# Performance work log

Measured on AMD Instinct MI355X. Metric: run time of the kernel, lower is better.

## Reference

```python
import jax, jax.numpy as jnp
import numpy as np
import math

D = 32   # in_planes / d_model
T = 9    # num_contexts
L = 24   # token_len
H = 8    # nhead
HD = D // H
NEUMANN = 3
ALPHA = 0.9

def _lin(x, w, b):
    return x @ w.T + b

def _gelu(x):
    return jax.nn.gelu(x, approximate=False)

def reference(x, ln_g, ln_b, rp_w1, rp_b1, rp_w2, rp_b2, W_causal,
              mask_w, mask_b, val_w1, val_b1, val_w2, val_b2, fuse_gate,
              q_w, q_b, k_w, k_b, v_w, v_b, m_w, m_b,
              W_logit, W_ctx, rel_pos_bias, pre_prompt, conv_w, conv_b, p_w, p_b):
    b = x.shape[0]
    x_btlc = jnp.transpose(x, (0, 2, 3, 1))              # (b,t,l,c)
    # ---- rule pooling (LayerNorm -> Linear -> GELU -> Linear) ----
    pooled = x_btlc.mean(axis=(1, 2))                    # (b,c)
    mu = pooled.mean(-1, keepdims=True)
    var = pooled.var(-1, keepdims=True)
    pn = (pooled - mu) / jnp.sqrt(var + 1e-5) * ln_g + ln_b
    pooled_rule = _lin(_gelu(_lin(pn, rp_w1, rp_b1)), rp_w2, rp_b2)
    # ---- causal graph discovery ----
    A = jax.nn.softplus(W_causal) * (1.0 - jnp.eye(D, dtype=x.dtype))
    # ---- intervention engine ----
    x_obs = x_btlc.mean(axis=(1, 2))                     # (b,c)
    scale = jnp.clip(jnp.std(x_btlc, axis=(1, 2), ddof=1), 1e-3)  # torch unbiased std
    M = jax.nn.sigmoid(_lin(pooled_rule, mask_w, mask_b))
    v_raw = _lin(_gelu(_lin(pooled_rule, val_w1, val_b1)), val_w2, val_b2)
    v32 = jnp.tanh(v_raw) * scale + x_obs
    x_do = (1.0 - M) * x_obs + M * v32
    A32 = ALPHA * A / (A.sum(-1, keepdims=True) + 1e-6)  # row-normalize
    y = x_do
    for _ in range(NEUMANN):                             # fp32 Neumann series
        y = x_do + y @ A32.T
    delta = (y - x_obs)[:, None, None, :]
    fused = x_btlc + jax.nn.sigmoid(fuse_gate) * delta   # (b,t,l,c)
    # ---- cosine-sim multi-head attention with rel-pos bias & head mixing ----
    def heads(w, bb):
        h = _lin(fused, w, bb).reshape(b, T, L, H, HD).transpose(0, 1, 3, 2, 4)
        return h / jnp.linalg.norm(h, axis=-1, keepdims=True).clip(1e-12)
    q = heads(q_w, q_b); k = heads(k_w, k_b); v = heads(v_w, v_b)
    logits = jnp.einsum('bthid,bthjd->bthij', q, k) / math.sqrt(HD)
    idx = jnp.arange(L)
    rel = jnp.clip(idx[:, None] - idx[None, :] + (L - 1), 0, 2 * L - 2)
    logits = logits + rel_pos_bias[:, rel][None, None]   # (h,L,L) broadcast
    logits = jnp.einsum('bthij,hH->btHij', logits, W_logit)
    atten = jax.nn.softmax(logits, axis=-1)
    atten = jnp.einsum('bthij,hH->btHij', atten, W_ctx)
    x_att = jnp.einsum('bthij,bthjd->bthid', atten, v)
    x_att = _lin(x_att.transpose(0, 1, 3, 2, 4).reshape(b, T, L, D), m_w, m_b)
    x_att = jnp.transpose(x_att, (0, 3, 1, 2))           # (b,c,t,l)
    # ---- prediction branch (conv over contexts + linear over tokens) ----
    pre = jnp.broadcast_to(pre_prompt, (b, D, 1, L))
    con = jnp.concatenate([x_att[:, :, :T - 1], pre], axis=2)   # (b,c,T,L)
    p = jax.lax.conv_general_dilated(con, conv_w, (1, 1), 'VALID',
        dimension_numbers=('NCHW', 'OIHW', 'NCHW')) + conv_b[None, :, None, None]
    p = jax.nn.relu(p)                                   # ConvNormAct act; norm=identity at init
    p = _lin(p, p_w, p_b)                                # Linear(token_len, token_len)
    p = x_att[:, :, T - 1:] - p
    return jnp.concatenate([x_att[:, :, :T - 1], p], axis=2)


def setup_inputs() -> dict:
    key = jax.random.key(0)
    ks = jax.random.split(key, 24)
    B = 4096
    def r(i, sh, s=0.02):
        return jax.random.normal(ks[i], sh, jnp.float32) * s
    return dict(
        x=jax.random.normal(ks[0], (B, D, T, L), jnp.float32),
        ln_g=jnp.ones((D,), jnp.float32), ln_b=jnp.zeros((D,), jnp.float32),
        rp_w1=r(1, (D, D)), rp_b1=jnp.zeros((D,), jnp.float32),
        rp_w2=r(2, (D, D)), rp_b2=jnp.zeros((D,), jnp.float32),
        W_causal=r(3, (D, D)),
        mask_w=r(4, (D, D)), mask_b=jnp.zeros((D,), jnp.float32),
        val_w1=r(5, (D, D)), val_b1=jnp.zeros((D,), jnp.float32),
        val_w2=r(6, (D, D)), val_b2=jnp.zeros((D,), jnp.float32),
        fuse_gate=jnp.float32(0.5),
        q_w=r(7, (D, D)), q_b=jnp.zeros((D,), jnp.float32),
        k_w=r(8, (D, D)), k_b=jnp.zeros((D,), jnp.float32),
        v_w=r(9, (D, D)), v_b=jnp.zeros((D,), jnp.float32),
        m_w=r(10, (D, D)), m_b=jnp.zeros((D,), jnp.float32),
        W_logit=jnp.eye(H, dtype=jnp.float32) + r(11, (H, H), 0.01),
        W_ctx=jnp.eye(H, dtype=jnp.float32) + r(12, (H, H), 0.01),
        rel_pos_bias=r(13, (H, 2 * L - 1)),
        pre_prompt=r(14, (1, D, 1, L)),
        conv_w=r(15, (D, D, T, 1)), conv_b=jnp.zeros((D,), jnp.float32),
        p_w=r(16, (L, L)), p_b=jnp.zeros((L,), jnp.float32),
    )
```

## Files before the change

kernel.cpp:

```cpp
#include <hip/hip_runtime.h>
#include <hip/hip_bf16.h>

#define DD 32
#define TT 9
#define LL 24
#define HH 8
#define NPOS 216
#define RPB_W 47
#define ALPHA 0.9f

__device__ __forceinline__ float gelu_exact(float x) {
    return 0.5f * x * (1.0f + erff(x * 0.7071067811865476f));
}
__device__ __forceinline__ float sigmoidf_(float x) { return 1.0f / (1.0f + expf(-x)); }


__global__ void k0_prep(const float* __restrict__ wcausal,
                        const float* __restrict__ w_logit,
                        const float* __restrict__ rpb,
                        float* __restrict__ ws) {
    __shared__ float A[DD][DD];
    __shared__ float rs[DD];
    int tid = threadIdx.x;
    int i = tid >> 5, j = tid & 31;
    float a = (i == j) ? 0.0f : log1pf(expf(wcausal[tid]));
    A[i][j] = a;
    __syncthreads();
    if (j == 0) {
        float s = 0.0f;
        for (int k = 0; k < DD; k++) s += A[i][k];
        rs[i] = ALPHA / (s + 1e-6f);
    }
    __syncthreads();
    ws[tid] = A[i][j] * rs[i];
    if (tid < 64) ws[1024 + tid] = 0.5f * w_logit[tid];
    if (tid < 384) {
        int H = tid / 48, r = tid % 48;
        float v = 0.0f;
        if (r < RPB_W) {
            for (int h = 0; h < HH; h++) v += w_logit[h * HH + H] * rpb[h * RPB_W + r];
        }
        ws[1088 + tid] = v;
    }
}

__global__ __launch_bounds__(256) void k1a(const float* __restrict__ x,
                                           float* __restrict__ sp, float* __restrict__ sq) {
    int b = blockIdx.x, tid = threadIdx.x;
    int c = tid >> 3, r = tid & 7;
    const float4* x4 = (const float4*)(x + (size_t)b * (DD * NPOS) + (size_t)c * NPOS);
    float s = 0.0f, q = 0.0f;
    for (int k = r; k < 54; k += 8) {
        float4 v = x4[k];
        s += v.x + v.y + v.z + v.w;
        q += v.x * v.x + v.y * v.y + v.z * v.z + v.w * v.w;
    }
    for (int m = 1; m < 8; m <<= 1) { s += __shfl_xor(s, m); q += __shfl_xor(q, m); }
    if (r == 0) { sp[b * DD + c] = s; sq[b * DD + c] = q; }
}

__global__ __launch_bounds__(64) void k1b(
    const float* __restrict__ ln_g, const float* __restrict__ ln_b,
    const float* __restrict__ rp_w1, const float* __restrict__ rp_b1,
    const float* __restrict__ rp_w2, const float* __restrict__ rp_b2,
    const float* __restrict__ mask_w, const float* __restrict__ mask_b,
    const float* __restrict__ val_w1, const float* __restrict__ val_b1,
    const float* __restrict__ val_w2, const float* __restrict__ val_b2,
    const float* __restrict__ fuse_gate, const float* __restrict__ ws,
    float* __restrict__ sp , const float* __restrict__ sq)
{
    __shared__ float W[6][1024];
    __shared__ float V[7][32];
    int tid = threadIdx.x;
    for (int idx = tid; idx < 1024; idx += 64) {
        W[0][idx] = rp_w1[idx]; W[1][idx] = rp_w2[idx]; W[2][idx] = mask_w[idx];
        W[3][idx] = val_w1[idx]; W[4][idx] = val_w2[idx]; W[5][idx] = ws[idx];
    }
    if (tid < 32) {
        V[0][tid] = ln_g[tid]; V[1][tid] = ln_b[tid]; V[2][tid] = rp_b1[tid];
        V[3][tid] = rp_b2[tid]; V[4][tid] = mask_b[tid]; V[5][tid] = val_b1[tid];
        V[6][tid] = val_b2[tid];
    }
    __syncthreads();
    int b = blockIdx.x * 64 + tid;

    float pooled[32], scl[32];
    const float4* sp4 = (const float4*)(sp + (size_t)b * 32);
    const float4* sq4 = (const float4*)(sq + (size_t)b * 32);
    #pragma unroll
    for (int k = 0; k < 8; k++) {
        float4 sv = sp4[k], qv = sq4[k];
        float ss[4] = {sv.x, sv.y, sv.z, sv.w};
        float qq[4] = {qv.x, qv.y, qv.z, qv.w};
        #pragma unroll
        for (int m = 0; m < 4; m++) {
            int c = 4 * k + m;
            float p = ss[m] * (1.0f / NPOS);
            pooled[c] = p;
            float var1 = (qq[m] - (float)NPOS * p * p) * (1.0f / (NPOS - 1));
            scl[c] = fmaxf(sqrtf(fmaxf(var1, 0.0f)), 1e-3f);
        }
    }
    float mu = 0.0f;
    #pragma unroll
    for (int c = 0; c < 32; c++) mu += pooled[c];
    mu *= (1.0f / 32.0f);
    float vv = 0.0f;
    #pragma unroll
    for (int c = 0; c < 32; c++) { float d = pooled[c] - mu; vv += d * d; }
    vv *= (1.0f / 32.0f);
    float inv = rsqrtf(vv + 1e-5f);
    float pn[32];
    #pragma unroll
    for (int c = 0; c < 32; c++) pn[c] = (pooled[c] - mu) * inv * V[0][c] + V[1][c];

    float h1[32];
    #pragma unroll
    for (int i = 0; i < 32; i++) {
        float acc = V[2][i];
        #pragma unroll
        for (int j = 0; j < 32; j++) acc += pn[j] * W[0][i * 32 + j];
        h1[i] = gelu_exact(acc);
    }
    float pr[32];
    #pragma unroll
    for (int i = 0; i < 32; i++) {
        float acc = V[3][i];
        #pragma unroll
        for (int j = 0; j < 32; j++) acc += h1[j] * W[1][i * 32 + j];
        pr[i] = acc;
    }
    float g1[32];
    #pragma unroll
    for (int i = 0; i < 32; i++) {
        float acc = V[5][i];
        #pragma unroll
        for (int j = 0; j < 32; j++) acc += pr[j] * W[3][i * 32 + j];
        g1[i] = gelu_exact(acc);
    }
    float xd[32];
    #pragma unroll
    for (int i = 0; i < 32; i++) {
        float am = V[4][i];
        #pragma unroll
        for (int j = 0; j < 32; j++) am += pr[j] * W[2][i * 32 + j];
        float M = sigmoidf_(am);
        float av = V[6][i];
        #pragma unroll
        for (int j = 0; j < 32; j++) av += g1[j] * W[4][i * 32 + j];
        float v32 = tanhf(av) * scl[i] + pooled[i];
        xd[i] = (1.0f - M) * pooled[i] + M * v32;
    }
    float y[32];
    #pragma unroll
    for (int c = 0; c < 32; c++) y[c] = xd[c];
    for (int it = 0; it < 3; it++) {
        float ny[32];
        #pragma unroll
        for (int i = 0; i < 32; i++) {
            float acc = xd[i];
            #pragma unroll
            for (int j = 0; j < 32; j++) acc += y[j] * W[5][i * 32 + j];
            ny[i] = acc;
        }
        #pragma unroll
        for (int c = 0; c < 32; c++) y[c] = ny[c];
    }
    float g = sigmoidf_(fuse_gate[0]);
    float4* dout4 = (float4*)(sp + (size_t)b * 32);
    #pragma unroll
    for (int k = 0; k < 8; k++) {
        float4 o;
        o.x = g * (y[4 * k + 0] - pooled[4 * k + 0]);
        o.y = g * (y[4 * k + 1] - pooled[4 * k + 1]);
        o.z = g * (y[4 * k + 2] - pooled[4 * k + 2]);
        o.w = g * (y[4 * k + 3] - pooled[4 * k + 3]);
        dout4[k] = o;
    }
}

__global__ __launch_bounds__(256) void k2_attn(
    const float* __restrict__ x,
    const float* __restrict__ ws,
    const float* __restrict__ delta,
    const float* __restrict__ q_w, const float* __restrict__ q_b,
    const float* __restrict__ k_w, const float* __restrict__ k_b,
    const float* __restrict__ v_w, const float* __restrict__ v_b,
    const float* __restrict__ m_w, const float* __restrict__ m_b,
    const float* __restrict__ w_ctx,
    float* __restrict__ out)
{
    __shared__ float r1[3456];
    __shared__ float r2[5824];
    __shared__ float msc[640];
    float* fusedf = r1;
    float* qsf = r1 + 864;
    float* ksf = r1 + 1728;
    float* vsf = r1 + 2592;
    float* wqf = r2;
    float* wkf = r2 + 1024;
    float* wvf = r2 + 2048;
    float* lgf = r2;
    float* wmf = r2 + 4800;
    float* bqf = msc, *bkf = msc + 32, *bvf = msc + 64, *bmf = msc + 96;
    float* wl05f = msc + 128;
    float* wcf = msc + 192;
    float* rpmf = msc + 256;

    int blk = blockIdx.x;
    int b = blk / TT, t = blk % TT;
    int tid = threadIdx.x;

    for (int idx = tid; idx < 768; idx += 256) {
        int m = idx >> 8, r = idx & 255;
        int i = r >> 3, jq = r & 7;
        const float* src = (m == 0) ? q_w : (m == 1) ? k_w : v_w;
        float* dst = (m == 0) ? wqf : (m == 1) ? wkf : wvf;
        float4 v = ((const float4*)src)[r];
        int col = i ^ (4 * jq);
        dst[(4 * jq + 0) * 32 + col] = v.x;
        dst[(4 * jq + 1) * 32 + col] = v.y;
        dst[(4 * jq + 2) * 32 + col] = v.z;
        dst[(4 * jq + 3) * 32 + col] = v.w;
    }
    if (tid < 32) { bqf[tid] = q_b[tid]; bkf[tid] = k_b[tid]; bvf[tid] = v_b[tid]; bmf[tid] = m_b[tid]; }
    else if (tid < 96) wl05f[tid - 32] = ws[1024 + tid - 32];
    else if (tid < 160) wcf[tid - 96] = w_ctx[tid - 96];
    for (int idx = tid; idx < 384; idx += 256) rpmf[idx] = ws[1088 + idx];
    if (tid < 192) {
        int c = tid / 6, k = tid % 6;
        const float4* p = (const float4*)(x + (size_t)b * (DD * NPOS) + (size_t)c * NPOS + t * LL);
        float4 v = p[k];
        float gd = delta[b * DD + c];
        int l0 = 4 * k;
        fusedf[(l0 + 0) * 36 + c] = v.x + gd;
        fusedf[(l0 + 1) * 36 + c] = v.y + gd;
        fusedf[(l0 + 2) * 36 + c] = v.z + gd;
        fusedf[(l0 + 3) * 36 + c] = v.w + gd;
    }
    __syncthreads();

    if (tid < 192) {
        int l = tid >> 3, q = tid & 7;
        float4 aq = *(const float4*)&bqf[4 * q];
        float4 ak = *(const float4*)&bkf[4 * q];
        float4 av = *(const float4*)&bvf[4 * q];
        #pragma unroll
        for (int j = 0; j < 32; j++) {
            float f = fusedf[l * 36 + j];
            int sw = (4 * q) ^ (j & 28);
            float4 w0 = *(const float4*)&wqf[j * 32 + sw];
            float4 w1 = *(const float4*)&wkf[j * 32 + sw];
            float4 w2 = *(const float4*)&wvf[j * 32 + sw];
            aq.x += f * w0.x; aq.y += f * w0.y; aq.z += f * w0.z; aq.w += f * w0.w;
            ak.x += f * w1.x; ak.y += f * w1.y; ak.z += f * w1.z; ak.w += f * w1.w;
            av.x += f * w2.x; av.y += f * w2.y; av.z += f * w2.z; av.w += f * w2.w;
        }
        float nq = 1.0f / fmaxf(sqrtf(aq.x*aq.x + aq.y*aq.y + aq.z*aq.z + aq.w*aq.w), 1e-12f);
        float nk = 1.0f / fmaxf(sqrtf(ak.x*ak.x + ak.y*ak.y + ak.z*ak.z + ak.w*ak.w), 1e-12f);
        float nv = 1.0f / fmaxf(sqrtf(av.x*av.x + av.y*av.y + av.z*av.z + av.w*av.w), 1e-12f);
        aq.x *= nq; aq.y *= nq; aq.z *= nq; aq.w *= nq;
        ak.x *= nk; ak.y *= nk; ak.z *= nk; ak.w *= nk;
        av.x *= nv; av.y *= nv; av.z *= nv; av.w *= nv;
        *(float4*)&qsf[l * 36 + 4 * q] = aq;
        *(float4*)&ksf[l * 36 + 4 * q] = ak;
        *(float4*)&vsf[l * 36 + 4 * q] = av;
    }
    __syncthreads();

    {
        int idx = tid;
        int i = idx >> 3, jq = idx & 7;
        float4 v = ((const float4*)m_w)[idx];
        int col = i ^ (4 * jq);
        wmf[(4 * jq + 0) * 32 + col] = v.x;
        wmf[(4 * jq + 1) * 32 + col] = v.y;
        wmf[(4 * jq + 2) * 32 + col] = v.z;
        wmf[(4 * jq + 3) * 32 + col] = v.w;
    }
    if (tid < 192) {
        int h = tid & 7, i2 = tid >> 3;
        float4 q4 = *(const float4*)&qsf[i2 * 36 + 4 * h];
        float row[24];
        #pragma unroll
        for (int j = 0; j < 24; j++) {
            float4 k4 = *(const float4*)&ksf[j * 36 + 4 * h];
            row[j] = q4.x * k4.x + q4.y * k4.y + q4.z * k4.z + q4.w * k4.w;
        }
        #pragma unroll
        for (int j = 0; j < 24; j++) lgf[h * 600 + i2 * 25 + j] = row[j];
    }
    __syncthreads();

    for (int ij = tid; ij < 576; ij += 256) {
        int i = ij / 24, j = ij - i * 24;
        int off = i * 25 + j;
        int rel = i - j + (LL - 1);
        float tmp[8];
        #pragma unroll
        for (int h = 0; h < 8; h++) tmp[h] = lgf[h * 600 + off];
        #pragma unroll
        for (int H = 0; H < 8; H++) {
            float a = rpmf[H * 48 + rel];
            #pragma unroll
            for (int h = 0; h < 8; h++) a += tmp[h] * wl05f[h * 8 + H];
            lgf[H * 600 + off] = a;
        }
    }
    __syncthreads();

    if (tid < 192) {
        int H = tid & 7, i = tid >> 3;
        float* rp = &lgf[H * 600 + i * 25];
        float mx = -1e30f;
        #pragma unroll
        for (int j = 0; j < 24; j++) mx = fmaxf(mx, rp[j]);
        float s = 0.0f;
        #pragma unroll
        for (int j = 0; j < 24; j++) { float e = __expf(rp[j] - mx); rp[j] = e; s += e; }
        float inv = 1.0f / s;
        #pragma unroll
        for (int j = 0; j < 24; j++) rp[j] *= inv;
    }
    __syncthreads();

    for (int ij = tid; ij < 576; ij += 256) {
        int i = ij / 24, j = ij - i * 24;
        int off = i * 25 + j;
        float tmp[8];
        #pragma unroll
        for (int h = 0; h < 8; h++) tmp[h] = lgf[h * 600 + off];
        #pragma unroll
        for (int H = 0; H < 8; H++) {
            float a = 0.0f;
            #pragma unroll
            for (int h = 0; h < 8; h++) a += tmp[h] * wcf[h * 8 + H];
            lgf[H * 600 + off] = a;
        }
    }
    __syncthreads();

    if (tid < 192) {
        int l = tid >> 3, q = tid & 7;
        float4 acc = {0.0f, 0.0f, 0.0f, 0.0f};
        #pragma unroll
        for (int j = 0; j < 24; j++) {
            float a = lgf[q * 600 + l * 25 + j];
            float4 v4 = *(const float4*)&vsf[j * 36 + 4 * q];
            acc.x += a * v4.x; acc.y += a * v4.y; acc.z += a * v4.z; acc.w += a * v4.w;
        }
        *(float4*)&fusedf[l * 36 + 4 * q] = acc;
    }
    __syncthreads();

    if (tid < 192) {
        int l = tid >> 3, q = tid & 7;
        float4 acc = *(const float4*)&bmf[4 * q];
        #pragma unroll
        for (int c = 0; c < 32; c++) {
            float f = fusedf[l * 36 + c];
            int sw = (4 * q) ^ (c & 28);
            float4 w4 = *(const float4*)&wmf[c * 32 + sw];
            acc.x += f * w4.x; acc.y += f * w4.y; acc.z += f * w4.z; acc.w += f * w4.w;
        }
        float* resf = qsf;
        resf[(4 * q + 0) * 25 + l] = acc.x;
        resf[(4 * q + 1) * 25 + l] = acc.y;
        resf[(4 * q + 2) * 25 + l] = acc.z;
        resf[(4 * q + 3) * 25 + l] = acc.w;
    }
    __syncthreads();

    if (tid < 192) {
        const float* resf = qsf;
        int c = tid / 6, k = tid - c * 6;
        float4 v;
        v.x = resf[c * 25 + 4 * k + 0];
        v.y = resf[c * 25 + 4 * k + 1];
        v.z = resf[c * 25 + 4 * k + 2];
        v.w = resf[c * 25 + 4 * k + 3];
        float4* o4 = (float4*)(out + (size_t)b * (DD * NPOS) + (size_t)c * NPOS + t * LL);
        o4[k] = v;
    }
}

__global__ __launch_bounds__(256) void k3_pred(
    const float* __restrict__ pre_prompt,
    const float* __restrict__ conv_w, const float* __restrict__ conv_b,
    const float* __restrict__ p_w, const float* __restrict__ p_b,
    float* __restrict__ out)
{
    __shared__ float conf[DD * NPOS];
    __shared__ __hip_bfloat16 cwh[DD * 324];
    __shared__ float pbuff[DD * 25];
    __shared__ __hip_bfloat16 pwh[24 * 28];
    __shared__ float pbv[24], cbv[32];
    int b = blockIdx.x, tid = threadIdx.x;

    const float4* o4 = (const float4*)(out + (size_t)b * (DD * NPOS));
    for (int idx = tid; idx < 1728; idx += 256) {
        int flat = idx * 4;
        int t = (flat % NPOS) / LL;
        float4 v;
        if (t < 8) {
            v = o4[idx];
        } else {
            int c = flat / NPOS, l = flat % LL;
            v = ((const float4*)pre_prompt)[(c * LL + l) >> 2];
        }
        *(float4*)&conf[flat] = v;
    }
    for (int idx = tid; idx < 2304; idx += 256) {
        float4 v = ((const float4*)conv_w)[idx];
        int flat = idx * 4;
        float vv[4] = {v.x, v.y, v.z, v.w};
        #pragma unroll
        for (int e = 0; e < 4; e++) {
            int f = flat + e;
            int co = f / 288, r = f - co * 288;
            int ci = r / 9, ttt = r - ci * 9;
            cwh[co * 324 + ci * 10 + ttt] = __float2bfloat16(vv[e]);
        }
    }
    for (int idx = tid; idx < 144; idx += 256) {
        float4 v = ((const float4*)p_w)[idx];
        int flat = idx * 4;
        float vv[4] = {v.x, v.y, v.z, v.w};
        #pragma unroll
        for (int e = 0; e < 4; e++) {
            int f = flat + e;
            int row = f / 24, col = f - row * 24;
            pwh[row * 28 + col] = __float2bfloat16(vv[e]);
        }
    }
    if (tid < 24) pbv[tid] = p_b[tid];
    if (tid >= 32 && tid < 64) cbv[tid - 32] = conv_b[tid - 32];
    __syncthreads();

    if (tid < 192) {
        int co = tid / 6, ql = tid - co * 6;
        float cb = cbv[co];
        float4 acc = {cb, cb, cb, cb};
        const float4* cf4 = (const float4*)conf;
        for (int ci = 0; ci < 32; ci++) {
            const uint32_t* wp = (const uint32_t*)&cwh[co * 324 + ci * 10];
            #pragma unroll
            for (int p = 0; p < 4; p++) {
                uint32_t u = wp[p];
                float w0 = __uint_as_float(u << 16);
                float w1 = __uint_as_float(u & 0xffff0000u);
                float4 v0 = cf4[ci * 54 + (2 * p) * 6 + ql];
                float4 v1 = cf4[ci * 54 + (2 * p + 1) * 6 + ql];
                acc.x += w0 * v0.x + w1 * v1.x;
                acc.y += w0 * v0.y + w1 * v1.y;
                acc.z += w0 * v0.z + w1 * v1.z;
                acc.w += w0 * v0.w + w1 * v1.w;
            }
            float w8 = __bfloat162float(cwh[co * 324 + ci * 10 + 8]);
            float4 v8 = cf4[ci * 54 + 48 + ql];
            acc.x += w8 * v8.x; acc.y += w8 * v8.y; acc.z += w8 * v8.z; acc.w += w8 * v8.w;
        }
        pbuff[co * 25 + 4 * ql + 0] = fmaxf(acc.x, 0.0f);
        pbuff[co * 25 + 4 * ql + 1] = fmaxf(acc.y, 0.0f);
        pbuff[co * 25 + 4 * ql + 2] = fmaxf(acc.z, 0.0f);
        pbuff[co * 25 + 4 * ql + 3] = fmaxf(acc.w, 0.0f);
    }
    __syncthreads();

    if (tid < 192) {
        int c = tid / 6, ql = tid - c * 6;
        float accv[4] = {pbv[4 * ql + 0], pbv[4 * ql + 1], pbv[4 * ql + 2], pbv[4 * ql + 3]};
        #pragma unroll
        for (int lp = 0; lp < 24; lp += 2) {
            float pv0 = pbuff[c * 25 + lp];
            float pv1 = pbuff[c * 25 + lp + 1];
            #pragma unroll
            for (int e = 0; e < 4; e++) {
                uint32_t u = *(const uint32_t*)&pwh[(4 * ql + e) * 28 + lp];
                accv[e] += pv0 * __uint_as_float(u << 16) + pv1 * __uint_as_float(u & 0xffff0000u);
            }
        }
        float4* op = (float4*)(out + (size_t)b * (DD * NPOS) + (size_t)c * NPOS + 8 * LL);
        float4 xa = op[ql];
        float4 r;
        r.x = xa.x - accv[0]; r.y = xa.y - accv[1]; r.z = xa.z - accv[2]; r.w = xa.w - accv[3];
        op[ql] = r;
    }
}

extern "C" void kernel_launch(void* const* d_in, const int* in_sizes, int n_in,
                              void* d_out, int out_size, void* d_ws, size_t ws_size,
                              hipStream_t stream) {
    const float* x        = (const float*)d_in[0];
    const float* ln_g     = (const float*)d_in[1];
    const float* ln_b     = (const float*)d_in[2];
    const float* rp_w1    = (const float*)d_in[3];
    const float* rp_b1    = (const float*)d_in[4];
    const float* rp_w2    = (const float*)d_in[5];
    const float* rp_b2    = (const float*)d_in[6];
    const float* W_causal = (const float*)d_in[7];
    const float* mask_w   = (const float*)d_in[8];
    const float* mask_b   = (const float*)d_in[9];
    const float* val_w1   = (const float*)d_in[10];
    const float* val_b1   = (const float*)d_in[11];
    const float* val_w2   = (const float*)d_in[12];
    const float* val_b2   = (const float*)d_in[13];
    const float* fuse_g   = (const float*)d_in[14];
    const float* q_w      = (const float*)d_in[15];
    const float* q_b      = (const float*)d_in[16];
    const float* k_w      = (const float*)d_in[17];
    const float* k_b      = (const float*)d_in[18];
    const float* v_w      = (const float*)d_in[19];
    const float* v_b      = (const float*)d_in[20];
    const float* m_w      = (const float*)d_in[21];
    const float* m_b      = (const float*)d_in[22];
    const float* W_logit  = (const float*)d_in[23];
    const float* W_ctx    = (const float*)d_in[24];
    const float* rel_pb   = (const float*)d_in[25];
    const float* pre_pr   = (const float*)d_in[26];
    const float* conv_w   = (const float*)d_in[27];
    const float* conv_b   = (const float*)d_in[28];
    const float* p_w      = (const float*)d_in[29];
    const float* p_b      = (const float*)d_in[30];
    float* out = (float*)d_out;

    int B = in_sizes[0] / (DD * NPOS);

    float* ws = (float*)d_ws;
    float* sp = ws + 2048;
    float* sq = sp + (size_t)B * 32;

    hipLaunchKernelGGL(k0_prep, dim3(1), dim3(1024), 0, stream, W_causal, W_logit, rel_pb, ws);
    hipLaunchKernelGGL(k1a, dim3(B), dim3(256), 0, stream, x, sp, sq);
    hipLaunchKernelGGL(k1b, dim3(B / 64), dim3(64), 0, stream,
                       ln_g, ln_b, rp_w1, rp_b1, rp_w2, rp_b2,
                       mask_w, mask_b, val_w1, val_b1, val_w2, val_b2,
                       fuse_g, ws, sp, sq);
    hipLaunchKernelGGL(k2_attn, dim3(B * TT), dim3(256), 0, stream,
                       x, ws, sp, q_w, q_b, k_w, k_b, v_w, v_b, m_w, m_b,
                       W_ctx, out);
    hipLaunchKernelGGL(k3_pred, dim3(B), dim3(256), 0, stream,
                       pre_pr, conv_w, conv_b, p_w, p_b, out);
}
```

Baseline: 1.019 ms.

## Fuse head-mixing, softmax and context mixing into register passes with head-interleaved logits

Stores the attention logits with the head index innermost, so each row's eight heads can be read as two float4 loads. The logit head-mix, rel-pos bias and softmax are fused into one register-resident pass per thread, and the context head-mix is folded into the attention-times-V loop. This removes two full shared-memory passes and their barriers. The Q/K/V and output projections also switch to float4 loads of the fused input. The trade-off is a 24-float register array per thread and the context mix being recomputed inside the AV loop.

After: 989.4 us. -2.9%, faster.

```diff
diff --git a/kernel.cpp b/kernel.cpp
--- a/kernel.cpp
+++ b/kernel.cpp
@@ -200,7 +200,7 @@
     float* wqf = r2;
     float* wkf = r2 + 1024;
     float* wvf = r2 + 2048;
-    float* lgf = r2;
+    float* lg2 = r2;
     float* wmf = r2 + 4800;
     float* bqf = msc, *bkf = msc + 32, *bvf = msc + 64, *bmf = msc + 96;
     float* wl05f = msc + 128;
@@ -246,15 +246,21 @@
         float4 ak = *(const float4*)&bkf[4 * q];
         float4 av = *(const float4*)&bvf[4 * q];
         #pragma unroll
-        for (int j = 0; j < 32; j++) {
-            float f = fusedf[l * 36 + j];
-            int sw = (4 * q) ^ (j & 28);
-            float4 w0 = *(const float4*)&wqf[j * 32 + sw];
-            float4 w1 = *(const float4*)&wkf[j * 32 + sw];
-            float4 w2 = *(const float4*)&wvf[j * 32 + sw];
-            aq.x += f * w0.x; aq.y += f * w0.y; aq.z += f * w0.z; aq.w += f * w0.w;
-            ak.x += f * w1.x; ak.y += f * w1.y; ak.z += f * w1.z; ak.w += f * w1.w;
-            av.x += f * w2.x; av.y += f * w2.y; av.z += f * w2.z; av.w += f * w2.w;
+        for (int jq = 0; jq < 8; jq++) {
+            float4 f4 = *(const float4*)&fusedf[l * 36 + 4 * jq];
+            float fv[4] = {f4.x, f4.y, f4.z, f4.w};
+            #pragma unroll
+            for (int jj = 0; jj < 4; jj++) {
+                int j = 4 * jq + jj;
+                int sw = (4 * q) ^ (j & 28);
+                float f = fv[jj];
+                float4 w0 = *(const float4*)&wqf[j * 32 + sw];
+                float4 w1 = *(const float4*)&wkf[j * 32 + sw];
+                float4 w2 = *(const float4*)&wvf[j * 32 + sw];
+                aq.x += f * w0.x; aq.y += f * w0.y; aq.z += f * w0.z; aq.w += f * w0.w;
+                ak.x += f * w1.x; ak.y += f * w1.y; ak.z += f * w1.z; ak.w += f * w1.w;
+                av.x += f * w2.x; av.y += f * w2.y; av.z += f * w2.z; av.w += f * w2.w;
+            }
         }
         float nq = 1.0f / fmaxf(sqrtf(aq.x*aq.x + aq.y*aq.y + aq.z*aq.z + aq.w*aq.w), 1e-12f);
         float nk = 1.0f / fmaxf(sqrtf(ak.x*ak.x + ak.y*ak.y + ak.z*ak.z + ak.w*ak.w), 1e-12f);
@@ -288,64 +294,56 @@
             row[j] = q4.x * k4.x + q4.y * k4.y + q4.z * k4.z + q4.w * k4.w;
         }
         #pragma unroll
-        for (int j = 0; j < 24; j++) lgf[h * 600 + i2 * 25 + j] = row[j];
-    }
-    __syncthreads();
-
-    for (int ij = tid; ij < 576; ij += 256) {
-        int i = ij / 24, j = ij - i * 24;
-        int off = i * 25 + j;
-        int rel = i - j + (LL - 1);
-        float tmp[8];
-        #pragma unroll
-        for (int h = 0; h < 8; h++) tmp[h] = lgf[h * 600 + off];
-        #pragma unroll
-        for (int H = 0; H < 8; H++) {
-            float a = rpmf[H * 48 + rel];
-            #pragma unroll
-            for (int h = 0; h < 8; h++) a += tmp[h] * wl05f[h * 8 + H];
-            lgf[H * 600 + off] = a;
-        }
-    }
-    __syncthreads();
-
-    if (tid < 192) {
-        int H = tid & 7, i = tid >> 3;
-        float* rp = &lgf[H * 600 + i * 25];
-        float mx = -1e30f;
-        #pragma unroll
-        for (int j = 0; j < 24; j++) mx = fmaxf(mx, rp[j]);
-        float s = 0.0f;
-        #pragma unroll
-        for (int j = 0; j < 24; j++) { float e = __expf(rp[j] - mx); rp[j] = e; s += e; }
-        float inv = 1.0f / s;
-        #pragma unroll
-        for (int j = 0; j < 24; j++) rp[j] *= inv;
-    }
-    __syncthreads();
-
-    for (int ij = tid; ij < 576; ij += 256) {
-        int i = ij / 24, j = ij - i * 24;
-        int off = i * 25 + j;
-        float tmp[8];
-        #pragma unroll
-        for (int h = 0; h < 8; h++) tmp[h] = lgf[h * 600 + off];
-        #pragma unroll
-        for (int H = 0; H < 8; H++) {
-            float a = 0.0f;
-            #pragma unroll
-            for (int h = 0; h < 8; h++) a += tmp[h] * wcf[h * 8 + H];
-            lgf[H * 600 + off] = a;
+        for (int j = 0; j < 24; j++) lg2[i2 * 196 + j * 8 + h] = row[j];
+    }
+    __syncthreads();
+
+    float sm[24];
+    {
+        if (tid < 192) {
+            int H = tid & 7, i = tid >> 3;
+            float wlc[8];
+            #pragma unroll
+            for (int h = 0; h < 8; h++) wlc[h] = wl05f[h * 8 + H];
+            float mx = -1e30f;
+            #pragma unroll
+            for (int j = 0; j < 24; j++) {
+                float4 ta = *(const float4*)&lg2[i * 196 + j * 8];
+                float4 tb = *(const float4*)&lg2[i * 196 + j * 8 + 4];
+                float a = rpmf[H * 48 + (i - j + 23)];
+                a += ta.x * wlc[0] + ta.y * wlc[1] + ta.z * wlc[2] + ta.w * wlc[3]
+                   + tb.x * wlc[4] + tb.y * wlc[5] + tb.z * wlc[6] + tb.w * wlc[7];
+                sm[j] = a;
+                mx = fmaxf(mx, a);
+            }
+            float s = 0.0f;
+            #pragma unroll
+            for (int j = 0; j < 24; j++) { float e = __expf(sm[j] - mx); sm[j] = e; s += e; }
+            float inv = 1.0f / s;
+            #pragma unroll
+            for (int j = 0; j < 24; j++) sm[j] *= inv;
+        }
+        __syncthreads();
+        if (tid < 192) {
+            int H = tid & 7, i = tid >> 3;
+            #pragma unroll
+            for (int j = 0; j < 24; j++) lg2[i * 196 + j * 8 + H] = sm[j];
         }
     }
     __syncthreads();
 
     if (tid < 192) {
         int l = tid >> 3, q = tid & 7;
+        float wcc[8];
+        #pragma unroll
+        for (int h = 0; h < 8; h++) wcc[h] = wcf[h * 8 + q];
         float4 acc = {0.0f, 0.0f, 0.0f, 0.0f};
         #pragma unroll
         for (int j = 0; j < 24; j++) {
-            float a = lgf[q * 600 + l * 25 + j];
+            float4 ta = *(const float4*)&lg2[l * 196 + j * 8];
+            float4 tb = *(const float4*)&lg2[l * 196 + j * 8 + 4];
+            float a = ta.x * wcc[0] + ta.y * wcc[1] + ta.z * wcc[2] + ta.w * wcc[3]
+                    + tb.x * wcc[4] + tb.y * wcc[5] + tb.z * wcc[6] + tb.w * wcc[7];
             float4 v4 = *(const float4*)&vsf[j * 36 + 4 * q];
             acc.x += a * v4.x; acc.y += a * v4.y; acc.z += a * v4.z; acc.w += a * v4.w;
         }
@@ -357,11 +355,17 @@
         int l = tid >> 3, q = tid & 7;
         float4 acc = *(const float4*)&bmf[4 * q];
         #pragma unroll
-        for (int c = 0; c < 32; c++) {
-            float f = fusedf[l * 36 + c];
-            int sw = (4 * q) ^ (c & 28);
-            float4 w4 = *(const float4*)&wmf[c * 32 + sw];
-            acc.x += f * w4.x; acc.y += f * w4.y; acc.z += f * w4.z; acc.w += f * w4.w;
+        for (int cq = 0; cq < 8; cq++) {
+            float4 f4 = *(const float4*)&fusedf[l * 36 + 4 * cq];
+            float fv[4] = {f4.x, f4.y, f4.z, f4.w};
+            #pragma unroll
+            for (int cc = 0; cc < 4; cc++) {
+                int c = 4 * cq + cc;
+                int sw = (4 * q) ^ (c & 28);
+                float f = fv[cc];
+                float4 w4 = *(const float4*)&wmf[c * 32 + sw];
+                acc.x += f * w4.x; acc.y += f * w4.y; acc.z += f * w4.z; acc.w += f * w4.w;
+            }
         }
         float* resf = qsf;
         resf[(4 * q + 0) * 25 + l] = acc.x;
```
